# Kernel tuning notes

Measured on AMD Instinct MI355X. Metric: run time of the kernel, lower is better.

The kernel has to match this reference:

```python
import jax, jax.numpy as jnp
import numpy as np

# static architecture constants
NUM_GRAPHS = 64
NODES_PER_GRAPH = 512
N_TOTAL = NUM_GRAPHS * NODES_PER_GRAPH          # 32768
AVG_DEG = 16
E_TOTAL = N_TOTAL * AVG_DEG                      # 524288
NODE_NUMBER = 1000
EMB = 128
DIMF = 128
NUM_LAYERS = 4
K = 64
DIM_TARGET = 2
LATENT = NUM_LAYERS * DIMF + 1                   # 513


def setup_inputs() -> dict:
    key = jax.random.key(0)
    ks = jax.random.split(key, 16)
    # node ids
    x = jax.random.randint(ks[0], (N_TOTAL,), 0, NODE_NUMBER, dtype=jnp.int32)
    # edges confined within each graph
    epg = NODES_PER_GRAPH * AVG_DEG
    src_l = jax.random.randint(ks[1], (NUM_GRAPHS, epg), 0, NODES_PER_GRAPH, dtype=jnp.int32)
    dst_l = jax.random.randint(ks[2], (NUM_GRAPHS, epg), 0, NODES_PER_GRAPH, dtype=jnp.int32)
    off = (jnp.arange(NUM_GRAPHS, dtype=jnp.int32) * NODES_PER_GRAPH)[:, None]
    edge_index = jnp.stack([(src_l + off).reshape(-1), (dst_l + off).reshape(-1)])  # [2,E]
    batch = jnp.repeat(jnp.arange(NUM_GRAPHS, dtype=jnp.int32), NODES_PER_GRAPH)

    def lin(k, fi, fo):
        return jax.random.normal(k, (fi, fo), jnp.float32) / np.sqrt(fi)

    emb = jax.random.normal(ks[3], (NODE_NUMBER, EMB), jnp.float32)
    W_convs = jnp.stack([lin(jax.random.fold_in(ks[4], l), EMB if l == 0 else DIMF, DIMF)
                         for l in range(NUM_LAYERS)])            # [L,128,128]
    b_convs = jnp.zeros((NUM_LAYERS, DIMF), jnp.float32)
    W_last = lin(ks[5], DIMF, 1)
    b_last = jnp.zeros((1,), jnp.float32)
    conv1_w = jax.random.normal(ks[6], (16, 1, LATENT), jnp.float32) / np.sqrt(LATENT)
    conv1_b = jnp.zeros((16,), jnp.float32)
    conv2_w = jax.random.normal(ks[7], (32, 16, 5), jnp.float32) / np.sqrt(16 * 5)
    conv2_b = jnp.zeros((32,), jnp.float32)
    dd = (K - 2) // 2 + 1                      # 32
    in_dense = (dd - 5 + 1) * 32               # 896
    d1_w = lin(ks[8], in_dense, dd)
    d1_b = jnp.zeros((dd,), jnp.float32)
    d2_w = lin(ks[9], dd, DIM_TARGET)
    d2_b = jnp.zeros((DIM_TARGET,), jnp.float32)
    return dict(x=x, edge_index=edge_index, batch=batch, emb=emb,
                W_convs=W_convs, b_convs=b_convs, W_last=W_last, b_last=b_last,
                conv1_w=conv1_w, conv1_b=conv1_b, conv2_w=conv2_w, conv2_b=conv2_b,
                d1_w=d1_w, d1_b=d1_b, d2_w=d2_w, d2_b=d2_b)


def _gcn(h, W, b, src, dst, norm):
    # linear -> gather -> degree-normalize -> scatter-add (DGCNNConv with aggr='add')
    h = h @ W + b
    msg = h[src] * norm[:, None]
    return jax.ops.segment_sum(msg, dst, num_segments=N_TOTAL)


def reference(x, edge_index, batch, emb, W_convs, b_convs, W_last, b_last,
              conv1_w, conv1_b, conv2_w, conv2_b, d1_w, d1_b, d2_w, d2_b):
    loops = jnp.arange(N_TOTAL, dtype=edge_index.dtype)
    src = jnp.concatenate([edge_index[0], loops])
    dst = jnp.concatenate([edge_index[1], loops])
    # deg = degree(src); norm = deg^-1 gathered at dst (as in DGCNNConv.message)
    deg = jax.ops.segment_sum(jnp.ones_like(src, jnp.float32), src, num_segments=N_TOTAL)
    norm = (1.0 / deg)[dst]

    h = emb[x]                                           # [N,128]
    hidden = []
    for l in range(NUM_LAYERS):
        h = jnp.tanh(_gcn(h, W_convs[l], b_convs[l], src, dst, norm))
        hidden.append(h)
    h = jnp.tanh(_gcn(h, W_last, b_last, src, dst, norm))  # [N,1]
    hidden.append(h)
    xcat = jnp.concatenate(hidden, axis=1)               # [N, 513]

    # global_sort_pool: batch is sorted with equal-size graphs -> dense reshape
    x3 = xcat.reshape(NUM_GRAPHS, NODES_PER_GRAPH, LATENT)
    order = jnp.argsort(-x3[..., -1], axis=1)[:, :K]     # descending by last channel, top-k
    pooled = jnp.take_along_axis(x3, order[:, :, None], axis=1)  # [B,K,513]

    # conv1d(1,16,kernel=513,stride=513) over [B,1,K*513] == per-row projection
    y1 = jax.nn.relu(jnp.einsum('bkd,od->bok', pooled, conv1_w[:, 0, :])
                     + conv1_b[None, :, None])           # [B,16,K]
    L = K // 2
    y1 = y1.reshape(NUM_GRAPHS, 16, L, 2).max(axis=-1)   # maxpool(2,2)
    y2 = jax.lax.conv_general_dilated(y1, conv2_w, (1,), 'VALID',
                                      dimension_numbers=('NCH', 'OIH', 'NCH'))
    y2 = jax.nn.relu(y2 + conv2_b[None, :, None])        # [B,32,L-4]
    flat = y2.reshape(NUM_GRAPHS, -1)                    # [B,896]
    h1 = jax.nn.relu(flat @ d1_w + d1_b)                 # dropout is identity in eval
    logits = h1 @ d2_w + d2_b
    return jax.nn.softmax(logits, axis=-1)
```

## Files before the change

kernel.cpp:

```cpp
#include <hip/hip_runtime.h>
#include <hip/hip_bf16.h>
#include <math.h>

#define N_TOTAL 32768
#define E_TOTAL 524288
#define NUM_GRAPHS 64
#define NPG 512
#define EMB 128
#define MAXD 64
#define KTOP 64
#define LATENT 513
#define PPAD 524

typedef __attribute__((ext_vector_type(8))) short bf16x8;
typedef __attribute__((ext_vector_type(4))) float f32x4;

__device__ __forceinline__ unsigned short f2bf(float f) {
    unsigned u = __float_as_uint(f);
    return (unsigned short)((u + 0x7FFFu + ((u >> 16) & 1u)) >> 16);
}
__device__ __forceinline__ float bf2f(unsigned short h) {
    return __uint_as_float(((unsigned)h) << 16);
}


__global__ __launch_bounds__(256) void k_init(int* __restrict__ deg, int* __restrict__ cnt) {
    int i = blockIdx.x * 256 + threadIdx.x;
    if (i < N_TOTAL) { deg[i] = 1; cnt[i] = 0; }
}

__global__ __launch_bounds__(256) void k_build(const int* __restrict__ ei,
                                               int* __restrict__ deg, int* __restrict__ cnt,
                                               int* __restrict__ adj) {
    int e = blockIdx.x * 256 + threadIdx.x;
    if (e >= E_TOTAL) return;
    int s = ei[e];
    int d = ei[E_TOTAL + e];
    atomicAdd(&deg[s], 1);
    int slot = atomicAdd(&cnt[d], 1);
    if (slot < MAXD) adj[(size_t)d * MAXD + slot] = s;
}


__global__ __launch_bounds__(256) void k_prep(const float* __restrict__ Wc,
                                              unsigned short* __restrict__ Wth,
                                              unsigned short* __restrict__ Wtl) {
    __shared__ float tile[64][65];
    int b = blockIdx.x;
    int l = b >> 2, t = b & 3;
    int k0 = (t >> 1) * 64, o0 = (t & 1) * 64;
    int lane = threadIdx.x & 63, q = threadIdx.x >> 6;
    const float* Wsrc = Wc + (size_t)l * 16384;
#pragma unroll
    for (int it = 0; it < 16; ++it) {
        int r = it * 4 + q;
        tile[r][lane] = Wsrc[(size_t)(k0 + r) * 128 + o0 + lane];
    }
    __syncthreads();
#pragma unroll
    for (int it = 0; it < 16; ++it) {
        int o = it * 4 + q;
        float v = tile[lane][o];
        unsigned short h = f2bf(v);
        unsigned short lo = f2bf(v - bf2f(h));
        size_t dst = (size_t)l * 16384 + (size_t)(o0 + o) * 128 + k0 + lane;
        Wth[dst] = h; Wtl[dst] = lo;
    }
}


__global__ __launch_bounds__(256) void k_layer(const int* __restrict__ xids,
                                               const float* __restrict__ Hin,
                                               const unsigned short* __restrict__ Wth,
                                               const unsigned short* __restrict__ Wtl,
                                               const float* __restrict__ bvec,
                                               const float* __restrict__ Wl,
                                               const float* __restrict__ bl,
                                               float* __restrict__ tmp,
                                               float* __restrict__ Hout,
                                               const int* __restrict__ adj,
                                               const int* __restrict__ cnt,
                                               const int* __restrict__ deg) {
    __shared__ unsigned char smem[8192];
    __shared__ float lsum[16];
    int tid = threadIdx.x;
    int w = tid >> 6, lane = tid & 63;
    int bid = blockIdx.x;
    int xcd = bid & 7, j = bid >> 3;
    int g = (xcd << 3) + (j >> 5);
    int chunk = j & 31;
    int rowbase = g * NPG + chunk * 16;
    int wrow = rowbase + w * 4;
    const float2* h2 = (const float2*)Hin;

    int c4[4]; int nb4[4];
    float2 s0[4], s1[4], s2[4], s3[4];
#pragma unroll
    for (int p = 0; p < 4; ++p) {
        int v = wrow + p;
        int c = cnt[v]; if (c > MAXD) c = MAXD;
        c4[p] = c;
        const int* av = adj + (size_t)v * MAXD;
        int nb = (lane < c) ? av[lane] : 0;
        int iv = v;
        if (xids) {
            nb = (lane < c) ? xids[nb] : 0;
            iv = xids[v];
        }
        nb4[p] = nb;
        s0[p] = h2[(size_t)iv * 64 + lane];
        s1[p] = make_float2(0.f, 0.f);
        s2[p] = make_float2(0.f, 0.f);
        s3[p] = make_float2(0.f, 0.f);
    }
    int mx = max(max(c4[0], c4[1]), max(c4[2], c4[3]));
    for (int t = 0; t < mx; t += 4) {
#pragma unroll
        for (int p = 0; p < 4; ++p) if (t < c4[p]) {
            float2 v = h2[(size_t)__shfl(nb4[p], t) * 64 + lane];
            s0[p].x += v.x; s0[p].y += v.y;
        }
#pragma unroll
        for (int p = 0; p < 4; ++p) if (t + 1 < c4[p]) {
            float2 v = h2[(size_t)__shfl(nb4[p], t + 1) * 64 + lane];
            s1[p].x += v.x; s1[p].y += v.y;
        }
#pragma unroll
        for (int p = 0; p < 4; ++p) if (t + 2 < c4[p]) {
            float2 v = h2[(size_t)__shfl(nb4[p], t + 2) * 64 + lane];
            s2[p].x += v.x; s2[p].y += v.y;
        }
#pragma unroll
        for (int p = 0; p < 4; ++p) if (t + 3 < c4[p]) {
            float2 v = h2[(size_t)__shfl(nb4[p], t + 3) * 64 + lane];
            s3[p].x += v.x; s3[p].y += v.y;
        }
    }
#pragma unroll
    for (int p = 0; p < 4; ++p) {
        float2 s;
        s.x = (s0[p].x + s1[p].x) + (s2[p].x + s3[p].x);
        s.y = (s0[p].y + s1[p].y) + (s2[p].y + s3[p].y);
        int r = w * 4 + p;
        unsigned short hx = f2bf(s.x), hy = f2bf(s.y);
        unsigned short lx = f2bf(s.x - bf2f(hx)), ly = f2bf(s.y - bf2f(hy));
        int byte = r * 256 + ((lane * 4) ^ ((r & 7) << 4));
        *(unsigned*)(smem + byte)        = (unsigned)hx | ((unsigned)hy << 16);
        *(unsigned*)(smem + 4096 + byte) = (unsigned)lx | ((unsigned)ly << 16);
    }
    if (tid < 16) lsum[tid] = 0.f;
    __syncthreads();

    int r = lane & 15, kb = lane >> 4;
    bf16x8 ah[4], al[4];
#pragma unroll
    for (int ks = 0; ks < 4; ++ks) {
        int byte = r * 256 + ((ks * 64 + kb * 16) ^ ((r & 7) << 4));
        ah[ks] = *(const bf16x8*)(smem + byte);
        al[ks] = *(const bf16x8*)(smem + 4096 + byte);
    }
    float invd[4], cp1[4];
#pragma unroll
    for (int q = 0; q < 4; ++q) {
        int nd = rowbase + kb * 4 + q;
        invd[q] = 1.0f / (float)deg[nd];
        cp1[q]  = (float)(cnt[nd] + 1);
    }
    float z[4] = {0.f, 0.f, 0.f, 0.f};
#pragma unroll
    for (int cti = 0; cti < 2; ++cti) {
        int ct = w * 2 + cti;
        const unsigned short* Wh = Wth + (size_t)(ct * 16 + r) * 128;
        const unsigned short* Wo = Wtl + (size_t)(ct * 16 + r) * 128;
        f32x4 a = {0.f, 0.f, 0.f, 0.f};
#pragma unroll
        for (int ks = 0; ks < 4; ++ks) {
            bf16x8 wh = *(const bf16x8*)(Wh + ks * 32 + kb * 8);
            bf16x8 wl = *(const bf16x8*)(Wo + ks * 32 + kb * 8);
            a = __builtin_amdgcn_mfma_f32_16x16x32_bf16(ah[ks], wh, a, 0, 0, 0);
            a = __builtin_amdgcn_mfma_f32_16x16x32_bf16(ah[ks], wl, a, 0, 0, 0);
            a = __builtin_amdgcn_mfma_f32_16x16x32_bf16(al[ks], wh, a, 0, 0, 0);
        }
        float bcol = bvec[ct * 16 + r];
        float wlast = Wl ? Wl[ct * 16 + r] : 0.f;
#pragma unroll
        for (int q = 0; q < 4; ++q) {
            float val = tanhf((a[q] + bcol * cp1[q]) * invd[q]);
            Hout[(size_t)(rowbase + kb * 4 + q) * 128 + ct * 16 + r] = val;
            z[q] = fmaf(val, wlast, z[q]);
        }
    }
    if (Wl) {
#pragma unroll
        for (int m = 1; m < 16; m <<= 1) {
            z[0] += __shfl_xor(z[0], m); z[1] += __shfl_xor(z[1], m);
            z[2] += __shfl_xor(z[2], m); z[3] += __shfl_xor(z[3], m);
        }
        if (r == 0) {
#pragma unroll
            for (int q = 0; q < 4; ++q) atomicAdd(&lsum[kb * 4 + q], z[q]);
        }
        __syncthreads();
        if (tid < 16) tmp[rowbase + tid] = lsum[tid] + bl[0];
    }
}


__global__ __launch_bounds__(256) void k_sort(const float* __restrict__ tmp,
                                              const int* __restrict__ adj,
                                              const int* __restrict__ cnt,
                                              const int* __restrict__ deg,
                                              float* __restrict__ lastc,
                                              int* __restrict__ topk) {
    __shared__ float v[512];
    __shared__ int ix[512];
    int g = blockIdx.x, tid = threadIdx.x;
    for (int i = tid; i < 512; i += 256) {
        int node = g * NPG + i;
        float s = tmp[node];
        int c = cnt[node]; if (c > MAXD) c = MAXD;
        const int* av = adj + (size_t)node * MAXD;
#pragma unroll 4
        for (int q = 0; q < c; ++q) s += tmp[av[q]];
        float val = tanhf(s / (float)deg[node]);
        lastc[node] = val;
        v[i] = val; ix[i] = i;
    }
    __syncthreads();
    for (int ksz = 2; ksz <= 512; ksz <<= 1) {
        for (int jj = ksz >> 1; jj > 0; jj >>= 1) {
            for (int i = tid; i < 512; i += 256) {
                int p = i ^ jj;
                if (p > i) {
                    float va = v[i], vb = v[p];
                    int ia = ix[i], ib = ix[p];
                    bool b_before_a = (vb > va) || (vb == va && ib < ia);
                    bool up = (i & ksz) == 0;
                    bool sw = up ? b_before_a : !b_before_a;
                    if (sw) { v[i] = vb; v[p] = va; ix[i] = ib; ix[p] = ia; }
                }
            }
            __syncthreads();
        }
    }
    for (int k = tid; k < KTOP; k += 256) topk[g * KTOP + k] = g * NPG + ix[k];
}


__global__ __launch_bounds__(256) void k_conv1(const int* __restrict__ topk,
                                               const float* __restrict__ h0,
                                               const float* __restrict__ h1,
                                               const float* __restrict__ h2,
                                               const float* __restrict__ h3,
                                               const float* __restrict__ lastc,
                                               const float* __restrict__ c1w,
                                               const float* __restrict__ c1b,
                                               float* __restrict__ y1p) {
    __shared__ float P[16][PPAD];
    __shared__ float Y1c[16][16];
    __shared__ int nodes[16];
    int bid = blockIdx.x;
    int g = bid >> 2, cc = bid & 3;
    int tid = threadIdx.x;
    if (tid < 16) nodes[tid] = topk[g * KTOP + cc * 16 + tid];
    __syncthreads();

    {
        int r = tid >> 4, t4 = tid & 15;
        int node = nodes[r];
#pragma unroll
        for (int jj = 0; jj < 8; ++jj) {
            int d = (t4 + 16 * jj) * 4;
            const float* src = (d < 128) ? h0 : (d < 256) ? h1 : (d < 384) ? h2 : h3;
            float4 val = *(const float4*)(src + (size_t)node * 128 + (d & 127));
            *(float4*)&P[r][d] = val;
        }
        if (t4 == 0) P[r][512] = lastc[node];
    }
    __syncthreads();

    int o = tid >> 4, kk = tid & 15;
    const float* w = c1w + (size_t)o * LATENT;
    float a0 = 0.f, a1 = 0.f, a2 = 0.f, a3 = 0.f;
    for (int d = 0; d < 512; d += 4) {
        float4 p = *(const float4*)&P[kk][d];
        a0 = fmaf(p.x, w[d],     a0);
        a1 = fmaf(p.y, w[d + 1], a1);
        a2 = fmaf(p.z, w[d + 2], a2);
        a3 = fmaf(p.w, w[d + 3], a3);
    }
    float s = ((a0 + a1) + (a2 + a3)) + P[kk][512] * w[512] + c1b[o];
    Y1c[o][kk] = fmaxf(s, 0.f);
    __syncthreads();

    if (tid < 128) {
        int oo = tid >> 3, l = tid & 7;
        y1p[(size_t)g * 512 + oo * 32 + cc * 8 + l] = fmaxf(Y1c[oo][2 * l], Y1c[oo][2 * l + 1]);
    }
}


__global__ __launch_bounds__(256) void k_tail(const float* __restrict__ y1p,
                                              const float* __restrict__ c2w, const float* __restrict__ c2b,
                                              const float* __restrict__ d1w, const float* __restrict__ d1b,
                                              const float* __restrict__ d2w, const float* __restrict__ d2b,
                                              float* __restrict__ out) {
    __shared__ float Y1P[16][32];
    __shared__ float Y2[32][28];
    __shared__ float H1s[32];
    __shared__ float red[256];
    int g = blockIdx.x, tid = threadIdx.x;

    for (int t = tid; t < 512; t += 256) ((float*)Y1P)[t] = y1p[(size_t)g * 512 + t];
    __syncthreads();

    for (int t = tid; t < 32 * 28; t += 256) {
        int o2 = t / 28, tt = t - o2 * 28;
        float s = c2b[o2];
#pragma unroll
        for (int i = 0; i < 16; ++i)
#pragma unroll
            for (int dt = 0; dt < 5; ++dt)
                s = fmaf(Y1P[i][tt + dt], c2w[o2 * 80 + i * 5 + dt], s);
        Y2[o2][tt] = fmaxf(s, 0.f);
    }
    __syncthreads();

    {
        int jcol = tid >> 3, part = tid & 7;
        float s = 0.f;
        for (int rr = 0; rr < 4; ++rr) {
            int o2 = part * 4 + rr;
            int base = o2 * 28;
            for (int tt = 0; tt < 28; ++tt)
                s = fmaf(Y2[o2][tt], d1w[(size_t)(base + tt) * 32 + jcol], s);
        }
        red[tid] = s;
        __syncthreads();
        if (part == 0) {
            float t = 0.f;
#pragma unroll
            for (int p = 0; p < 8; ++p) t += red[tid + p];
            H1s[jcol] = fmaxf(t + d1b[jcol], 0.f);
        }
        __syncthreads();
    }

    if (tid == 0) {
        float l0 = d2b[0], l1 = d2b[1];
        for (int jc = 0; jc < 32; ++jc) {
            l0 = fmaf(H1s[jc], d2w[jc * 2 + 0], l0);
            l1 = fmaf(H1s[jc], d2w[jc * 2 + 1], l1);
        }
        float m = fmaxf(l0, l1);
        float e0 = expf(l0 - m), e1 = expf(l1 - m);
        float inv = 1.f / (e0 + e1);
        out[g * 2 + 0] = e0 * inv;
        out[g * 2 + 1] = e1 * inv;
    }
}


extern "C" void kernel_launch(void* const* d_in, const int* in_sizes, int n_in,
                              void* d_out, int out_size, void* d_ws, size_t ws_size,
                              hipStream_t stream) {
    const int*   x    = (const int*)d_in[0];
    const int*   ei   = (const int*)d_in[1];
    const float* emb  = (const float*)d_in[3];
    const float* Wc   = (const float*)d_in[4];
    const float* bc   = (const float*)d_in[5];
    const float* Wl   = (const float*)d_in[6];
    const float* bl   = (const float*)d_in[7];
    const float* c1w  = (const float*)d_in[8];
    const float* c1b  = (const float*)d_in[9];
    const float* c2w  = (const float*)d_in[10];
    const float* c2b  = (const float*)d_in[11];
    const float* d1w  = (const float*)d_in[12];
    const float* d1b  = (const float*)d_in[13];
    const float* d2w  = (const float*)d_in[14];
    const float* d2b  = (const float*)d_in[15];
    float* out = (float*)d_out;

    char* ws = (char*)d_ws;
    int*   deg  = (int*)ws;            ws += (size_t)N_TOTAL * 4;
    int*   cnt  = (int*)ws;            ws += (size_t)N_TOTAL * 4;
    int*   adj  = (int*)ws;            ws += (size_t)N_TOTAL * MAXD * 4;
    float* Hid0 = (float*)ws;          ws += (size_t)N_TOTAL * 128 * 4;
    float* Hid1 = (float*)ws;          ws += (size_t)N_TOTAL * 128 * 4;
    float* Hid2 = (float*)ws;          ws += (size_t)N_TOTAL * 128 * 4;
    float* Hid3 = (float*)ws;          ws += (size_t)N_TOTAL * 128 * 4;
    unsigned short* Wth = (unsigned short*)ws;  ws += (size_t)4 * 128 * 128 * 2;
    unsigned short* Wtl = (unsigned short*)ws;  ws += (size_t)4 * 128 * 128 * 2;
    float* tmp  = (float*)ws;          ws += (size_t)N_TOTAL * 4;
    float* lastc= (float*)ws;          ws += (size_t)N_TOTAL * 4;
    int*   topk = (int*)ws;            ws += (size_t)NUM_GRAPHS * KTOP * 4;
    float* y1p  = (float*)ws;          ws += (size_t)NUM_GRAPHS * 16 * 32 * 4;

    k_init <<<N_TOTAL / 256, 256, 0, stream>>>(deg, cnt);
    k_build<<<E_TOTAL / 256, 256, 0, stream>>>(ei, deg, cnt, adj);
    k_prep <<<16, 256, 0, stream>>>(Wc, Wth, Wtl);

    float* Hids[4] = {Hid0, Hid1, Hid2, Hid3};
    for (int l = 0; l < 4; ++l) {
        const int*   xl  = (l == 0) ? x : nullptr;
        const float* hin = (l == 0) ? emb : Hids[l - 1];
        const float* wl  = (l == 3) ? Wl : nullptr;
        const float* blp = (l == 3) ? bl : nullptr;
        float*       tp  = (l == 3) ? tmp : nullptr;
        k_layer<<<N_TOTAL / 16, 256, 0, stream>>>(xl, hin,
                                                  Wth + (size_t)l * 16384, Wtl + (size_t)l * 16384,
                                                  bc + (size_t)l * 128, wl, blp, tp,
                                                  Hids[l], adj, cnt, deg);
    }
    k_sort<<<NUM_GRAPHS, 256, 0, stream>>>(tmp, adj, cnt, deg, lastc, topk);
    k_conv1<<<NUM_GRAPHS * 4, 256, 0, stream>>>(topk, Hid0, Hid1, Hid2, Hid3, lastc, c1w, c1b, y1p);
    k_tail<<<NUM_GRAPHS, 256, 0, stream>>>(y1p, c2w, c2b, d1w, d1b, d2w, d2b, out);
}
```

Before: 365.2 us.

## Replace sparse neighbor gather with dense per-graph adjacency MFMA matmul

```diff
diff --git a/kernel.cpp b/kernel.cpp
--- a/kernel.cpp
+++ b/kernel.cpp
@@ -6,7 +6,6 @@
 #define E_TOTAL 524288
 #define NUM_GRAPHS 64
 #define NPG 512
-#define EMB 128
 #define MAXD 64
 #define KTOP 64
 #define LATENT 513
@@ -22,6 +21,9 @@
 __device__ __forceinline__ float bf2f(unsigned short h) {
     return __uint_as_float(((unsigned)h) << 16);
 }
+__device__ __forceinline__ int swz(int bir, int row) {
+    return (bir & ~127) | ((bir & 127) ^ ((row & 7) << 4));
+}
 
 
 __global__ __launch_bounds__(256) void k_init(int* __restrict__ deg, int* __restrict__ cnt) {
@@ -29,9 +31,13 @@
     if (i < N_TOTAL) { deg[i] = 1; cnt[i] = 0; }
 }
 
+__global__ __launch_bounds__(256) void k_zero(int4* __restrict__ p) {
+    p[(size_t)blockIdx.x * 256 + threadIdx.x] = make_int4(0, 0, 0, 0);
+}
+
 __global__ __launch_bounds__(256) void k_build(const int* __restrict__ ei,
                                                int* __restrict__ deg, int* __restrict__ cnt,
-                                               int* __restrict__ adj) {
+                                               int* __restrict__ adj, unsigned* __restrict__ Au) {
     int e = blockIdx.x * 256 + threadIdx.x;
     if (e >= E_TOTAL) return;
     int s = ei[e];
@@ -39,8 +45,30 @@
     atomicAdd(&deg[s], 1);
     int slot = atomicAdd(&cnt[d], 1);
     if (slot < MAXD) adj[(size_t)d * MAXD + slot] = s;
-}
-
+    int g = d >> 9, v = d & 511, u = s & 511;
+    atomicAdd(&Au[((size_t)g << 17) + (v << 8) + (u >> 1)], 1u << ((u & 1) << 4));
+}
+
+__global__ __launch_bounds__(256) void k_convA(const unsigned* __restrict__ Au,
+                                               unsigned short* __restrict__ Asw) {
+    size_t idx = (size_t)blockIdx.x * 256 + threadIdx.x;
+    size_t b4 = idx * 4;
+    int g = (int)(b4 >> 17);
+    int rem = (int)(b4 & 131071);
+    int v = rem >> 8;
+    int u0 = (rem & 255) * 2;
+    uint4 cw = *(const uint4*)(Au + b4);
+    unsigned r[4];
+#pragma unroll
+    for (int i = 0; i < 4; ++i) {
+        unsigned wv = (&cw.x)[i];
+        int ua = u0 + 2 * i, ub = ua + 1;
+        float ca = (float)(wv & 0xFFFFu) + ((ua == v) ? 1.f : 0.f);
+        float cb = (float)(wv >> 16)     + ((ub == v) ? 1.f : 0.f);
+        r[i] = (unsigned)f2bf(ca) | ((unsigned)f2bf(cb) << 16);
+    }
+    *(int4*)(Asw + ((size_t)g * 512 + v) * 512 + u0) = make_int4(r[0], r[1], r[2], r[3]);
+}
 
 __global__ __launch_bounds__(256) void k_prep(const float* __restrict__ Wc,
                                               unsigned short* __restrict__ Wth,
@@ -68,9 +96,49 @@
     }
 }
 
-
-__global__ __launch_bounds__(256) void k_layer(const int* __restrict__ xids,
-                                               const float* __restrict__ Hin,
+__global__ __launch_bounds__(256) void k_embT(const int* __restrict__ x,
+                                              const float* __restrict__ emb,
+                                              unsigned short* __restrict__ Ph,
+                                              unsigned short* __restrict__ Pl) {
+    __shared__ float P[64][132];
+    __shared__ int nodes[64];
+    int b = blockIdx.x;
+    int g = b >> 3, ck = b & 7;
+    int tid = threadIdx.x;
+    if (tid < 64) nodes[tid] = x[g * NPG + ck * 64 + tid];
+    __syncthreads();
+#pragma unroll
+    for (int c = 0; c < 8; ++c) {
+        int idx = tid + c * 256;
+        int row = idx >> 5, c4 = idx & 31;
+        float4 vv = *(const float4*)(emb + (size_t)nodes[row] * 128 + c4 * 4);
+        *(float4*)&P[row][c4 * 4] = vv;
+    }
+    __syncthreads();
+#pragma unroll
+    for (int c = 0; c < 4; ++c) {
+        int idx = tid + c * 256;
+        int ch = idx >> 3, grp = idx & 7;
+        unsigned hw[4], lw[4];
+#pragma unroll
+        for (int j = 0; j < 4; ++j) {
+            float a  = P[grp * 8 + 2 * j][ch];
+            float bq = P[grp * 8 + 2 * j + 1][ch];
+            unsigned short ha = f2bf(a),  hb = f2bf(bq);
+            unsigned short la = f2bf(a - bf2f(ha)), lb = f2bf(bq - bf2f(hb));
+            hw[j] = (unsigned)ha | ((unsigned)hb << 16);
+            lw[j] = (unsigned)la | ((unsigned)lb << 16);
+        }
+        size_t base = ((size_t)g * 128 + ch) * 512 + ck * 64 + grp * 8;
+        *(int4*)(Ph + base) = make_int4(hw[0], hw[1], hw[2], hw[3]);
+        *(int4*)(Pl + base) = make_int4(lw[0], lw[1], lw[2], lw[3]);
+    }
+}
+
+
+__global__ __launch_bounds__(256) void k_layer(const unsigned short* __restrict__ Ph,
+                                               const unsigned short* __restrict__ Pl,
+                                               const unsigned short* __restrict__ Asw,
                                                const unsigned short* __restrict__ Wth,
                                                const unsigned short* __restrict__ Wtl,
                                                const float* __restrict__ bvec,
@@ -78,86 +146,83 @@
                                                const float* __restrict__ bl,
                                                float* __restrict__ tmp,
                                                float* __restrict__ Hout,
-                                               const int* __restrict__ adj,
+                                               unsigned short* __restrict__ Poh,
+                                               unsigned short* __restrict__ Pol,
                                                const int* __restrict__ cnt,
                                                const int* __restrict__ deg) {
-    __shared__ unsigned char smem[8192];
-    __shared__ float lsum[16];
+    __shared__ char lds[40960];
     int tid = threadIdx.x;
     int w = tid >> 6, lane = tid & 63;
     int bid = blockIdx.x;
-    int xcd = bid & 7, j = bid >> 3;
-    int g = (xcd << 3) + (j >> 5);
-    int chunk = j & 31;
-    int rowbase = g * NPG + chunk * 16;
-    int wrow = rowbase + w * 4;
-    const float2* h2 = (const float2*)Hin;
-
-    int c4[4]; int nb4[4];
-    float2 s0[4], s1[4], s2[4], s3[4];
-#pragma unroll
-    for (int p = 0; p < 4; ++p) {
-        int v = wrow + p;
-        int c = cnt[v]; if (c > MAXD) c = MAXD;
-        c4[p] = c;
-        const int* av = adj + (size_t)v * MAXD;
-        int nb = (lane < c) ? av[lane] : 0;
-        int iv = v;
-        if (xids) {
-            nb = (lane < c) ? xids[nb] : 0;
-            iv = xids[v];
-        }
-        nb4[p] = nb;
-        s0[p] = h2[(size_t)iv * 64 + lane];
-        s1[p] = make_float2(0.f, 0.f);
-        s2[p] = make_float2(0.f, 0.f);
-        s3[p] = make_float2(0.f, 0.f);
-    }
-    int mx = max(max(c4[0], c4[1]), max(c4[2], c4[3]));
-    for (int t = 0; t < mx; t += 4) {
-#pragma unroll
-        for (int p = 0; p < 4; ++p) if (t < c4[p]) {
-            float2 v = h2[(size_t)__shfl(nb4[p], t) * 64 + lane];
-            s0[p].x += v.x; s0[p].y += v.y;
-        }
-#pragma unroll
-        for (int p = 0; p < 4; ++p) if (t + 1 < c4[p]) {
-            float2 v = h2[(size_t)__shfl(nb4[p], t + 1) * 64 + lane];
-            s1[p].x += v.x; s1[p].y += v.y;
-        }
-#pragma unroll
-        for (int p = 0; p < 4; ++p) if (t + 2 < c4[p]) {
-            float2 v = h2[(size_t)__shfl(nb4[p], t + 2) * 64 + lane];
-            s2[p].x += v.x; s2[p].y += v.y;
-        }
-#pragma unroll
-        for (int p = 0; p < 4; ++p) if (t + 3 < c4[p]) {
-            float2 v = h2[(size_t)__shfl(nb4[p], t + 3) * 64 + lane];
-            s3[p].x += v.x; s3[p].y += v.y;
-        }
-    }
-#pragma unroll
-    for (int p = 0; p < 4; ++p) {
-        float2 s;
-        s.x = (s0[p].x + s1[p].x) + (s2[p].x + s3[p].x);
-        s.y = (s0[p].y + s1[p].y) + (s2[p].y + s3[p].y);
-        int r = w * 4 + p;
-        unsigned short hx = f2bf(s.x), hy = f2bf(s.y);
-        unsigned short lx = f2bf(s.x - bf2f(hx)), ly = f2bf(s.y - bf2f(hy));
-        int byte = r * 256 + ((lane * 4) ^ ((r & 7) << 4));
-        *(unsigned*)(smem + byte)        = (unsigned)hx | ((unsigned)hy << 16);
-        *(unsigned*)(smem + 4096 + byte) = (unsigned)lx | ((unsigned)ly << 16);
-    }
-    if (tid < 16) lsum[tid] = 0.f;
-    __syncthreads();
-
+    int g = (bid & 7) * 8 + ((bid >> 3) & 7);
+    int vblk = bid >> 6;
+    int nodebase = g * NPG + vblk * 64;
     int r = lane & 15, kb = lane >> 4;
+
+    f32x4 acc[8];
+#pragma unroll
+    for (int n = 0; n < 8; ++n) acc[n] = (f32x4){0.f, 0.f, 0.f, 0.f};
+    size_t Abase = ((size_t)(g * NPG + vblk * 64)) * 512;
+    int vrow = w * 16 + r;
+
+    for (int kt = 0; kt < 8; ++kt) {
+#pragma unroll
+        for (int c = 0; c < 10; ++c) {
+            int idx = tid + c * 256;
+            const unsigned short* src;
+            int row, off16, ldsbase;
+            if (idx < 512)       { row = idx >> 3;          off16 = idx & 7;
+                src = Asw + Abase + (size_t)row * 512 + kt * 64 + off16 * 8;
+                ldsbase = 0; }
+            else if (idx < 1536) { int j = idx - 512;  row = j >> 3; off16 = j & 7;
+                src = Ph + ((size_t)g * 128 + row) * 512 + kt * 64 + off16 * 8;
+                ldsbase = 8192; }
+            else                 { int j = idx - 1536; row = j >> 3; off16 = j & 7;
+                src = Pl + ((size_t)g * 128 + row) * 512 + kt * 64 + off16 * 8;
+                ldsbase = 24576; }
+            int4 v = *(const int4*)src;
+            *(int4*)(lds + ldsbase + row * 128 + swz(off16 * 16, row)) = v;
+        }
+        __syncthreads();
+#pragma unroll
+        for (int s2 = 0; s2 < 2; ++s2) {
+            int bir = s2 * 64 + kb * 16;
+            bf16x8 aA = *(const bf16x8*)(lds + vrow * 128 + swz(bir, vrow));
+#pragma unroll
+            for (int n = 0; n < 8; ++n) {
+                int ch = n * 16 + r;
+                bf16x8 bh = *(const bf16x8*)(lds + 8192  + ch * 128 + swz(bir, ch));
+                bf16x8 bl2 = *(const bf16x8*)(lds + 24576 + ch * 128 + swz(bir, ch));
+                acc[n] = __builtin_amdgcn_mfma_f32_16x16x32_bf16(aA, bh,  acc[n], 0, 0, 0);
+                acc[n] = __builtin_amdgcn_mfma_f32_16x16x32_bf16(aA, bl2, acc[n], 0, 0, 0);
+            }
+        }
+        __syncthreads();
+    }
+
+#pragma unroll
+    for (int n = 0; n < 8; ++n) {
+#pragma unroll
+        for (int q = 0; q < 4; ++q) {
+            int v64 = w * 16 + kb * 4 + q;
+            int ch = n * 16 + r;
+            float s = acc[n][q];
+            unsigned short h = f2bf(s), lo = f2bf(s - bf2f(h));
+            int addr = v64 * 256 + swz(ch * 2, v64);
+            *(unsigned short*)(lds + 8192 + addr)  = h;
+            *(unsigned short*)(lds + 24576 + addr) = lo;
+        }
+    }
+    __syncthreads();
+
+    int rowbase = nodebase + w * 16;
     bf16x8 ah[4], al[4];
 #pragma unroll
     for (int ks = 0; ks < 4; ++ks) {
-        int byte = r * 256 + ((ks * 64 + kb * 16) ^ ((r & 7) << 4));
-        ah[ks] = *(const bf16x8*)(smem + byte);
-        al[ks] = *(const bf16x8*)(smem + 4096 + byte);
+        int v64 = w * 16 + r;
+        int addr = v64 * 256 + swz(ks * 64 + kb * 16, v64);
+        ah[ks] = *(const bf16x8*)(lds + 8192 + addr);
+        al[ks] = *(const bf16x8*)(lds + 24576 + addr);
     }
     float invd[4], cp1[4];
 #pragma unroll
@@ -167,9 +232,9 @@
         cp1[q]  = (float)(cnt[nd] + 1);
     }
     float z[4] = {0.f, 0.f, 0.f, 0.f};
-#pragma unroll
-    for (int cti = 0; cti < 2; ++cti) {
-        int ct = w * 2 + cti;
+    unsigned hiW[8][2], loW[8][2];
+#pragma unroll
+    for (int ct = 0; ct < 8; ++ct) {
         const unsigned short* Wh = Wth + (size_t)(ct * 16 + r) * 128;
         const unsigned short* Wo = Wtl + (size_t)(ct * 16 + r) * 128;
         f32x4 a = {0.f, 0.f, 0.f, 0.f};
@@ -183,13 +248,44 @@
         }
         float bcol = bvec[ct * 16 + r];
         float wlast = Wl ? Wl[ct * 16 + r] : 0.f;
+        unsigned short hq[4], lq[4];
 #pragma unroll
         for (int q = 0; q < 4; ++q) {
             float val = tanhf((a[q] + bcol * cp1[q]) * invd[q]);
             Hout[(size_t)(rowbase + kb * 4 + q) * 128 + ct * 16 + r] = val;
             z[q] = fmaf(val, wlast, z[q]);
-        }
-    }
+            hq[q] = f2bf(val);
+            lq[q] = f2bf(val - bf2f(hq[q]));
+        }
+        hiW[ct][0] = (unsigned)hq[0] | ((unsigned)hq[1] << 16);
+        hiW[ct][1] = (unsigned)hq[2] | ((unsigned)hq[3] << 16);
+        loW[ct][0] = (unsigned)lq[0] | ((unsigned)lq[1] << 16);
+        loW[ct][1] = (unsigned)lq[2] | ((unsigned)lq[3] << 16);
+    }
+
+    if (Poh) {
+        __syncthreads();
+#pragma unroll
+        for (int ct = 0; ct < 8; ++ct) {
+            int o = ct * 16 + r;
+            int v64 = w * 16 + kb * 4;
+            int addr = o * 128 + swz(v64 * 2, o);
+            *(int2*)(lds + addr)         = make_int2(hiW[ct][0], hiW[ct][1]);
+            *(int2*)(lds + 16384 + addr) = make_int2(loW[ct][0], loW[ct][1]);
+        }
+        __syncthreads();
+#pragma unroll
+        for (int c = 0; c < 8; ++c) {
+            int idx = tid + c * 256;
+            int arr = idx >> 10;
+            int j = idx & 1023;
+            int o = j >> 3, off16 = j & 7;
+            int4 v = *(const int4*)(lds + arr * 16384 + o * 128 + swz(off16 * 16, o));
+            unsigned short* dst = (arr ? Pol : Poh) + ((size_t)g * 128 + o) * 512 + vblk * 64 + off16 * 8;
+            *(int4*)dst = v;
+        }
+    }
+
     if (Wl) {
 #pragma unroll
         for (int m = 1; m < 16; m <<= 1) {
@@ -197,11 +293,10 @@
             z[2] += __shfl_xor(z[2], m); z[3] += __shfl_xor(z[3], m);
         }
         if (r == 0) {
-#pragma unroll
-            for (int q = 0; q < 4; ++q) atomicAdd(&lsum[kb * 4 + q], z[q]);
-        }
-        __syncthreads();
-        if (tid < 16) tmp[rowbase + tid] = lsum[tid] + bl[0];
+            float b0 = bl[0];
+#pragma unroll
+            for (int q = 0; q < 4; ++q) tmp[rowbase + kb * 4 + q] = z[q] + b0;
+        }
     }
 }
 
@@ -264,7 +359,6 @@
     int tid = threadIdx.x;
     if (tid < 16) nodes[tid] = topk[g * KTOP + cc * 16 + tid];
     __syncthreads();
-
     {
         int r = tid >> 4, t4 = tid & 15;
         int node = nodes[r];
@@ -278,7 +372,6 @@
         if (t4 == 0) P[r][512] = lastc[node];
     }
     __syncthreads();
-
     int o = tid >> 4, kk = tid & 15;
     const float* w = c1w + (size_t)o * LATENT;
     float a0 = 0.f, a1 = 0.f, a2 = 0.f, a3 = 0.f;
@@ -292,7 +385,6 @@
     float s = ((a0 + a1) + (a2 + a3)) + P[kk][512] * w[512] + c1b[o];
     Y1c[o][kk] = fmaxf(s, 0.f);
     __syncthreads();
-
     if (tid < 128) {
         int oo = tid >> 3, l = tid & 7;
         y1p[(size_t)g * 512 + oo * 32 + cc * 8 + l] = fmaxf(Y1c[oo][2 * l], Y1c[oo][2 * l + 1]);
@@ -310,10 +402,8 @@
     __shared__ float H1s[32];
     __shared__ float red[256];
     int g = blockIdx.x, tid = threadIdx.x;
-
     for (int t = tid; t < 512; t += 256) ((float*)Y1P)[t] = y1p[(size_t)g * 512 + t];
     __syncthreads();
-
     for (int t = tid; t < 32 * 28; t += 256) {
         int o2 = t / 28, tt = t - o2 * 28;
         float s = c2b[o2];
@@ -325,7 +415,6 @@
         Y2[o2][tt] = fmaxf(s, 0.f);
     }
     __syncthreads();
-
     {
         int jcol = tid >> 3, part = tid & 7;
         float s = 0.f;
@@ -345,7 +434,6 @@
         }
         __syncthreads();
     }
-
     if (tid == 0) {
         float l0 = d2b[0], l1 = d2b[1];
         for (int jc = 0; jc < 32; ++jc) {
@@ -395,24 +483,35 @@
     float* lastc= (float*)ws;          ws += (size_t)N_TOTAL * 4;
     int*   topk = (int*)ws;            ws += (size_t)NUM_GRAPHS * KTOP * 4;
     float* y1p  = (float*)ws;          ws += (size_t)NUM_GRAPHS * 16 * 32 * 4;
+    unsigned* Au = (unsigned*)ws;      ws += (size_t)NUM_GRAPHS * 512 * 256 * 4;
+    unsigned short* Asw = (unsigned short*)ws;  ws += (size_t)NUM_GRAPHS * 512 * 512 * 2;
+    unsigned short* PAh = (unsigned short*)ws;  ws += (size_t)NUM_GRAPHS * 128 * 512 * 2;
+    unsigned short* PAl = (unsigned short*)ws;  ws += (size_t)NUM_GRAPHS * 128 * 512 * 2;
+    unsigned short* PBh = (unsigned short*)ws;  ws += (size_t)NUM_GRAPHS * 128 * 512 * 2;
+    unsigned short* PBl = (unsigned short*)ws;  ws += (size_t)NUM_GRAPHS * 128 * 512 * 2;
 
     k_init <<<N_TOTAL / 256, 256, 0, stream>>>(deg, cnt);
-    k_build<<<E_TOTAL / 256, 256, 0, stream>>>(ei, deg, cnt, adj);
+    k_zero <<<8192, 256, 0, stream>>>((int4*)Au);
+    k_build<<<E_TOTAL / 256, 256, 0, stream>>>(ei, deg, cnt, adj, Au);
     k_prep <<<16, 256, 0, stream>>>(Wc, Wth, Wtl);
+    k_convA<<<8192, 256, 0, stream>>>(Au, Asw);
+    k_embT <<<NUM_GRAPHS * 8, 256, 0, stream>>>(x, emb, PAh, PAl);
 
     float* Hids[4] = {Hid0, Hid1, Hid2, Hid3};
+    unsigned short* Pin_h[4] = {PAh, PBh, PAh, PBh};
+    unsigned short* Pin_l[4] = {PAl, PBl, PAl, PBl};
+    unsigned short* Pout_h[4] = {PBh, PAh, PBh, nullptr};
+    unsigned short* Pout_l[4] = {PBl, PAl, PBl, nullptr};
     for (int l = 0; l < 4; ++l) {
-        const int*   xl  = (l == 0) ? x : nullptr;
-        const float* hin = (l == 0) ? emb : Hids[l - 1];
         const float* wl  = (l == 3) ? Wl : nullptr;
         const float* blp = (l == 3) ? bl : nullptr;
         float*       tp  = (l == 3) ? tmp : nullptr;
-        k_layer<<<N_TOTAL / 16, 256, 0, stream>>>(xl, hin,
-                                                  Wth + (size_t)l * 16384, Wtl + (size_t)l * 16384,
-                                                  bc + (size_t)l * 128, wl, blp, tp,
-                                                  Hids[l], adj, cnt, deg);
-    }
-    k_sort<<<NUM_GRAPHS, 256, 0, stream>>>(tmp, adj, cnt, deg, lastc, topk);
+        k_layer<<<512, 256, 0, stream>>>(Pin_h[l], Pin_l[l], Asw,
+                                         Wth + (size_t)l * 16384, Wtl + (size_t)l * 16384,
+                                         bc + (size_t)l * 128, wl, blp, tp,
+                                         Hids[l], Pout_h[l], Pout_l[l], cnt, deg);
+    }
+    k_sort <<<NUM_GRAPHS, 256, 0, stream>>>(tmp, adj, cnt, deg, lastc, topk);
     k_conv1<<<NUM_GRAPHS * 4, 256, 0, stream>>>(topk, Hid0, Hid1, Hid2, Hid3, lastc, c1w, c1b, y1p);
-    k_tail<<<NUM_GRAPHS, 256, 0, stream>>>(y1p, c2w, c2b, d1w, d1b, d2w, d2b, out);
-}
+    k_tail <<<NUM_GRAPHS, 256, 0, stream>>>(y1p, c2w, c2b, d1w, d1b, d2w, d2b, out);
+}
```

Result: slower. 407.0 us (+11.4%).
